# Performance work log

Hardware: AMD Instinct MI355X
Metric: run time of the kernel (lower is better)

## Reference

```python
import jax, jax.numpy as jnp
import numpy as np

BATCH = 8192
N = 32
A_NUM = 5
EPS = 1e-10
ALPHA = jnp.array([0.01, 0.25, 0.5, 0.9, 0.99], dtype=jnp.float32)


def setup_inputs() -> dict:
    key = jax.random.key(0)
    ks = jax.random.split(key, 9)
    stdv = 1.0 / np.sqrt(N)
    u = lambda k, shape: jax.random.uniform(k, shape, jnp.float32, -stdv, stdv)
    L = N * (N - 1) // 2
    return {
        "inputs": jax.random.normal(ks[0], (BATCH, N, N), jnp.float32),
        "state": jax.random.normal(ks[1], (BATCH, A_NUM * N * N), jnp.float32),
        "WR_root": u(ks[2], (A_NUM,)),
        "Wt_root": u(ks[3], (1,)),
        "Wphi_root": u(ks[4], (1,)),
        "Ws_root": u(ks[5], (A_NUM,)),
        "Br": u(ks[6], (L, 1)),
        "Bt": u(ks[7], (L, 1)),
        "By": u(ks[8], (L, 1)),
    }


def _skew(Bvec, n):
    # Replicates the torch loop: row 0 is zeros; row k (k>=1) gets B[k-1 : 2k-1]
    # in its first k columns (overlapping slices of the flat parameter vector).
    b = Bvec.reshape(-1)
    r = jnp.arange(n)[:, None]
    c = jnp.arange(n)[None, :]
    idx = jnp.clip(r - 1 + c, 0, b.shape[0] - 1)  # B[k-1+j] for entry (k, j)
    L = jnp.where(c < r, b[idx], jnp.zeros((), b.dtype))
    return L - L.T


def _cayley(S, n):
    # MatrixExp in the source: (I - S)^{-1} (I + S)
    I = jnp.eye(n, dtype=S.dtype)
    return jnp.linalg.solve(I - S, I + S)


def _translate(A, Bvec, n):
    # M @ A @ M.T with M the Cayley 'exp' of the skew matrix built from Bvec.
    M = _cayley(_skew(Bvec, n), n)
    return jnp.einsum('ij,bjk,lk->bil', M, A, M)


def _nus(W_root, A, eps):
    # Weighted average over the a_num axis with weights W_root^2 / (sum + eps).
    W = W_root * W_root
    return jnp.einsum('a,banm->bnm', W / (W.sum() + eps), A)


def reference(inputs, state, WR_root, Wt_root, Wphi_root, Ws_root, Br, Bt, By):
    Mt_1 = state.reshape(-1, A_NUM, N, N)                 # [B, a, n, n]
    X = inputs.reshape(BATCH, N, N)                       # [B, n, n]

    Yt = _nus(WR_root, Mt_1, EPS)                         # [B, n, n]
    Rt = _translate(Yt, Br, N)

    at = (Wt_root[0] ** 2) / ((Wt_root ** 2 + Wphi_root ** 2).sum() + EPS)
    Tt = (1.0 - at) * X + at * Rt                         # Frechet mean FM
    Phit = _translate(Tt, Bt, N)

    # Per-j Frechet means, vectorized over the a_num axis.
    a = ALPHA[None, :, None, None]
    Mt = (1.0 - a) * Mt_1 + a * Phit[:, None, :, :]       # [B, a, n, n]

    St = _nus(Ws_root, Mt, EPS)
    Ot = _translate(St, By, N)                            # [B, n, n]

    return Ot, Mt.reshape(-1, A_NUM, N, N)
```

## Files before the change

kernel.cpp:

```cpp
#include <hip/hip_runtime.h>

#define NB 8192
#define OT_ELEMS (NB * 1024)
#define EPSF 1e-10f

typedef __attribute__((ext_vector_type(4))) float f32x4;
typedef __attribute__((ext_vector_type(8))) short s16x8;

#define WAVE_FENCE() asm volatile("s_waitcnt lgkmcnt(0)" ::: "memory")
#define MFMA_B16(A, B, C) __builtin_amdgcn_mfma_f32_16x16x32_bf16((A), (B), (C), 0, 0, 0)

__global__ void cayley_kernel(const float* __restrict__ Br,
                              const float* __restrict__ Bt,
                              const float* __restrict__ By,
                              float* __restrict__ M_out) {
  __shared__ float A[32][33];
  __shared__ float R[32][33];
  const float* B = (blockIdx.x == 0) ? Br : (blockIdx.x == 1) ? Bt : By;
  const int t = threadIdx.x;
  const int i = t >> 5, j = t & 31;
  float Lij = (j < i) ? B[i - 1 + j] : 0.0f;
  float Lji = (i < j) ? B[j - 1 + i] : 0.0f;
  float S = Lij - Lji;
  float eye = (i == j) ? 1.0f : 0.0f;
  A[i][j] = eye - S;
  R[i][j] = eye + S;
  __syncthreads();
  for (int p = 0; p < 32; ++p) {
    float f = A[i][p] / A[p][p];
    __syncthreads();
    if (i != p) {
      A[i][j] -= f * A[p][j];
      R[i][j] -= f * R[p][j];
    }
    __syncthreads();
  }
  M_out[blockIdx.x * 1024 + i * 32 + j] = R[i][j] / A[i][i];
}

__device__ __forceinline__ void cvt_hilo8(const f32x4 f0, const f32x4 f1, s16x8& hi, s16x8& lo) {
  float f[8];
#pragma unroll
  for (int e = 0; e < 4; ++e) { f[e] = f0[e]; f[4 + e] = f1[e]; }
#pragma unroll
  for (int e = 0; e < 8; ++e) {
    unsigned u = __float_as_uint(f[e]);
    hi[e] = (short)(u >> 16);
    float ah = __uint_as_float(u & 0xffff0000u);
    lo[e] = (short)(__float_as_uint(f[e] - ah) >> 16);
  }
}

__device__ __forceinline__ void read_frag_lds(const float* sb, int off, s16x8& hi, s16x8& lo) {
  f32x4 f0 = *(const f32x4*)(sb + off);
  f32x4 f1 = *(const f32x4*)(sb + off + 4);
  cvt_hilo8(f0, f1, hi, lo);
}

__device__ __forceinline__ void congruence(float* sb, int lane,
                                           const s16x8 (&Mh)[2], const s16x8 (&Ml)[2],
                                           const f32x4 (&in)[2][2], f32x4 (&out)[2][2]) {
  const int l15 = lane & 15, l4 = lane >> 4;
#pragma unroll
  for (int ms = 0; ms < 2; ++ms)
#pragma unroll
    for (int ns = 0; ns < 2; ++ns)
      *(f32x4*)(sb + (16 * ns + l15) * 36 + 16 * ms + 4 * l4) = in[ms][ns];
  WAVE_FENCE();
  s16x8 Bh[2], Bl[2];
#pragma unroll
  for (int s = 0; s < 2; ++s)
    read_frag_lds(sb, (16 * s + l15) * 36 + 8 * l4, Bh[s], Bl[s]);
  WAVE_FENCE();
  f32x4 g[2][2];
#pragma unroll
  for (int ms = 0; ms < 2; ++ms)
#pragma unroll
    for (int ns = 0; ns < 2; ++ns) {
      f32x4 acc = {0.f, 0.f, 0.f, 0.f};
      acc = MFMA_B16(Ml[ms], Bh[ns], acc);
      acc = MFMA_B16(Mh[ms], Bl[ns], acc);
      acc = MFMA_B16(Mh[ms], Bh[ns], acc);
      g[ms][ns] = acc;
    }
#pragma unroll
  for (int ms = 0; ms < 2; ++ms)
#pragma unroll
    for (int ns = 0; ns < 2; ++ns)
#pragma unroll
      for (int r = 0; r < 4; ++r)
        sb[(16 * ms + 4 * l4 + r) * 36 + 16 * ns + l15] = g[ms][ns][r];
  WAVE_FENCE();
  s16x8 Ah[2], Al[2];
#pragma unroll
  for (int s = 0; s < 2; ++s)
    read_frag_lds(sb, (16 * s + l15) * 36 + 8 * l4, Ah[s], Al[s]);
  WAVE_FENCE();
#pragma unroll
  for (int ms = 0; ms < 2; ++ms)
#pragma unroll
    for (int ns = 0; ns < 2; ++ns) {
      f32x4 acc = {0.f, 0.f, 0.f, 0.f};
      acc = MFMA_B16(Al[ms], Mh[ns], acc);
      acc = MFMA_B16(Ah[ms], Ml[ns], acc);
      acc = MFMA_B16(Ah[ms], Mh[ns], acc);
      out[ms][ns] = acc;
    }
}

__global__ __launch_bounds__(64) void spdsru_main(
    const float* __restrict__ X, const float* __restrict__ state,
    const float* __restrict__ WR, const float* __restrict__ Wt,
    const float* __restrict__ Wphi, const float* __restrict__ Ws,
    const float* __restrict__ Mg, float* __restrict__ out) {
  __shared__ __align__(16) float sb[1152];
  const int lane = threadIdx.x;
  const int l15 = lane & 15, l4 = lane >> 4;
  const int batch = blockIdx.x;

  s16x8 Mh[3][2], Ml[3][2];
#pragma unroll
  for (int q = 0; q < 3; ++q)
#pragma unroll
    for (int s = 0; s < 2; ++s) {
      const float* p = Mg + q * 1024 + (16 * s + l15) * 32 + 8 * l4;
      cvt_hilo8(*(const f32x4*)p, *(const f32x4*)(p + 4), Mh[q][s], Ml[q][s]);
    }

  const float* xp = X + (size_t)batch * 1024;
  f32x4 x[2][2];
#pragma unroll
  for (int ms = 0; ms < 2; ++ms)
#pragma unroll
    for (int ns = 0; ns < 2; ++ns)
#pragma unroll
      for (int r = 0; r < 4; ++r)
        x[ms][ns][r] = xp[(16 * ms + 4 * l4 + r) * 32 + 16 * ns + l15];

  const float* stp = state + (size_t)batch * 5120;
  f32x4 m[5][2][2];
#pragma unroll
  for (int a = 0; a < 5; ++a)
#pragma unroll
    for (int ms = 0; ms < 2; ++ms)
#pragma unroll
      for (int ns = 0; ns < 2; ++ns)
#pragma unroll
        for (int r = 0; r < 4; ++r)
          m[a][ms][ns][r] = stp[a * 1024 + (16 * ms + 4 * l4 + r) * 32 + 16 * ns + l15];

  const float alpha[5] = {0.01f, 0.25f, 0.5f, 0.9f, 0.99f};
  float wr[5], wsn[5];
  {
    float sR = 0.f, sS = 0.f;
#pragma unroll
    for (int a = 0; a < 5; ++a) { float v = WR[a]; wr[a] = v * v; sR += v * v; }
#pragma unroll
    for (int a = 0; a < 5; ++a) { float v = Ws[a]; wsn[a] = v * v; sS += v * v; }
    const float invR = 1.0f / (sR + EPSF), invS = 1.0f / (sS + EPSF);
#pragma unroll
    for (int a = 0; a < 5; ++a) { wr[a] *= invR; wsn[a] *= invS; }
  }
  const float wt2 = Wt[0] * Wt[0], wp2 = Wphi[0] * Wphi[0];
  const float at = wt2 / (wt2 + wp2 + EPSF);
  const float omat = 1.0f - at;

  f32x4 U[2][2];
#pragma unroll
  for (int ms = 0; ms < 2; ++ms)
#pragma unroll
    for (int ns = 0; ns < 2; ++ns) {
      f32x4 u = wr[0] * m[0][ms][ns];
#pragma unroll
      for (int a = 1; a < 5; ++a) u += wr[a] * m[a][ms][ns];
      U[ms][ns] = u;
    }

  f32x4 rt[2][2];
  congruence(sb, lane, Mh[0], Ml[0], U, rt);

  f32x4 tt[2][2];
#pragma unroll
  for (int ms = 0; ms < 2; ++ms)
#pragma unroll
    for (int ns = 0; ns < 2; ++ns) tt[ms][ns] = omat * x[ms][ns] + at * rt[ms][ns];

  f32x4 ph[2][2];
  congruence(sb, lane, Mh[1], Ml[1], tt, ph);

  float* outMt = out + OT_ELEMS + (size_t)batch * 5120;
  f32x4 st[2][2];
#pragma unroll
  for (int ms = 0; ms < 2; ++ms)
#pragma unroll
    for (int ns = 0; ns < 2; ++ns) st[ms][ns] = f32x4{0.f, 0.f, 0.f, 0.f};
#pragma unroll
  for (int a = 0; a < 5; ++a) {
    const float al = alpha[a], om = 1.0f - al;
#pragma unroll
    for (int ms = 0; ms < 2; ++ms)
#pragma unroll
      for (int ns = 0; ns < 2; ++ns) {
        f32x4 mt = om * m[a][ms][ns] + al * ph[ms][ns];
        st[ms][ns] += wsn[a] * mt;
#pragma unroll
        for (int r = 0; r < 4; ++r)
          outMt[a * 1024 + (16 * ms + 4 * l4 + r) * 32 + 16 * ns + l15] = mt[r];
      }
  }

  f32x4 ot[2][2];
  congruence(sb, lane, Mh[2], Ml[2], st, ot);

  float* outOt = out + (size_t)batch * 1024;
#pragma unroll
  for (int ms = 0; ms < 2; ++ms)
#pragma unroll
    for (int ns = 0; ns < 2; ++ns)
#pragma unroll
      for (int r = 0; r < 4; ++r)
        outOt[(16 * ms + 4 * l4 + r) * 32 + 16 * ns + l15] = ot[ms][ns][r];
}

extern "C" void kernel_launch(void* const* d_in, const int* in_sizes, int n_in,
                              void* d_out, int out_size, void* d_ws, size_t ws_size,
                              hipStream_t stream) {
  const float* X     = (const float*)d_in[0];
  const float* state = (const float*)d_in[1];
  const float* WR    = (const float*)d_in[2];
  const float* Wt    = (const float*)d_in[3];
  const float* Wphi  = (const float*)d_in[4];
  const float* Ws    = (const float*)d_in[5];
  const float* Br    = (const float*)d_in[6];
  const float* Bt    = (const float*)d_in[7];
  const float* By    = (const float*)d_in[8];
  float* m_ws = (float*)d_ws;
  float* outp = (float*)d_out;

  cayley_kernel<<<3, 1024, 0, stream>>>(Br, Bt, By, m_ws);
  spdsru_main<<<NB, 64, 0, stream>>>(X, state, WR, Wt, Wphi, Ws, m_ws, outp);
}
```

Measured before the change: 104.9 us.

## Use 4x4 register tiles with vectorized global IO and fold St weights algebraically

Changes the per-lane ownership of each 32x32 matrix from the MFMA accumulator layout to a 4x4 tile, so global loads and stores become 16-byte vector accesses. The congruence routine now transposes through LDS on entry and exit to convert between this tile layout and the MFMA layout. The weighted sum St is rewritten as a precomputed weighted sum of the state plus a scalar times Phi. The state is read again from global memory in the Mt loop rather than kept in registers, which lowers register pressure but adds a second read and extra LDS round trips.

```diff
diff --git a/kernel.cpp b/kernel.cpp
--- a/kernel.cpp
+++ b/kernel.cpp
@@ -57,15 +57,16 @@
   cvt_hilo8(f0, f1, hi, lo);
 }
 
-__device__ __forceinline__ void congruence(float* sb, int lane,
-                                           const s16x8 (&Mh)[2], const s16x8 (&Ml)[2],
-                                           const f32x4 (&in)[2][2], f32x4 (&out)[2][2]) {
+__device__ __forceinline__ void congruence_rt(float* sb, int lane,
+                                              const s16x8 (&Mh)[2], const s16x8 (&Ml)[2],
+                                              const f32x4 (&in)[4], f32x4 (&outr)[4]) {
   const int l15 = lane & 15, l4 = lane >> 4;
-#pragma unroll
-  for (int ms = 0; ms < 2; ++ms)
-#pragma unroll
-    for (int ns = 0; ns < 2; ++ns)
-      *(f32x4*)(sb + (16 * ns + l15) * 36 + 16 * ms + 4 * l4) = in[ms][ns];
+  const int i0 = (lane >> 3) << 2, j0 = (lane & 7) << 2;
+#pragma unroll
+  for (int c = 0; c < 4; ++c) {
+    f32x4 colv = {in[0][c], in[1][c], in[2][c], in[3][c]};
+    *(f32x4*)(sb + (j0 + c) * 36 + i0) = colv;
+  }
   WAVE_FENCE();
   s16x8 Bh[2], Bl[2];
 #pragma unroll
@@ -96,6 +97,7 @@
   for (int s = 0; s < 2; ++s)
     read_frag_lds(sb, (16 * s + l15) * 36 + 8 * l4, Ah[s], Al[s]);
   WAVE_FENCE();
+  f32x4 o[2][2];
 #pragma unroll
   for (int ms = 0; ms < 2; ++ms)
 #pragma unroll
@@ -104,8 +106,20 @@
       acc = MFMA_B16(Al[ms], Mh[ns], acc);
       acc = MFMA_B16(Ah[ms], Ml[ns], acc);
       acc = MFMA_B16(Ah[ms], Mh[ns], acc);
-      out[ms][ns] = acc;
-    }
+      o[ms][ns] = acc;
+    }
+#pragma unroll
+  for (int ms = 0; ms < 2; ++ms)
+#pragma unroll
+    for (int ns = 0; ns < 2; ++ns)
+#pragma unroll
+      for (int r = 0; r < 4; ++r)
+        sb[(16 * ms + 4 * l4 + r) * 36 + 16 * ns + l15] = o[ms][ns][r];
+  WAVE_FENCE();
+#pragma unroll
+  for (int r = 0; r < 4; ++r)
+    outr[r] = *(const f32x4*)(sb + (i0 + r) * 36 + j0);
+  WAVE_FENCE();
 }
 
 __global__ __launch_bounds__(64) void spdsru_main(
@@ -116,6 +130,7 @@
   __shared__ __align__(16) float sb[1152];
   const int lane = threadIdx.x;
   const int l15 = lane & 15, l4 = lane >> 4;
+  const int i0 = (lane >> 3) << 2, j0 = (lane & 7) << 2;
   const int batch = blockIdx.x;
 
   s16x8 Mh[3][2], Ml[3][2];
@@ -127,99 +142,77 @@
       cvt_hilo8(*(const f32x4*)p, *(const f32x4*)(p + 4), Mh[q][s], Ml[q][s]);
     }
 
-  const float* xp = X + (size_t)batch * 1024;
-  f32x4 x[2][2];
-#pragma unroll
-  for (int ms = 0; ms < 2; ++ms)
-#pragma unroll
-    for (int ns = 0; ns < 2; ++ns)
-#pragma unroll
-      for (int r = 0; r < 4; ++r)
-        x[ms][ns][r] = xp[(16 * ms + 4 * l4 + r) * 32 + 16 * ns + l15];
-
-  const float* stp = state + (size_t)batch * 5120;
-  f32x4 m[5][2][2];
-#pragma unroll
-  for (int a = 0; a < 5; ++a)
-#pragma unroll
-    for (int ms = 0; ms < 2; ++ms)
-#pragma unroll
-      for (int ns = 0; ns < 2; ++ns)
-#pragma unroll
-        for (int r = 0; r < 4; ++r)
-          m[a][ms][ns][r] = stp[a * 1024 + (16 * ms + 4 * l4 + r) * 32 + 16 * ns + l15];
-
   const float alpha[5] = {0.01f, 0.25f, 0.5f, 0.9f, 0.99f};
-  float wr[5], wsn[5];
+  float wr[5], va[5];
+  float cP = 0.f;
   {
-    float sR = 0.f, sS = 0.f;
+    float sR = 0.f, sS = 0.f, wq[5];
 #pragma unroll
     for (int a = 0; a < 5; ++a) { float v = WR[a]; wr[a] = v * v; sR += v * v; }
 #pragma unroll
-    for (int a = 0; a < 5; ++a) { float v = Ws[a]; wsn[a] = v * v; sS += v * v; }
+    for (int a = 0; a < 5; ++a) { float v = Ws[a]; wq[a] = v * v; sS += v * v; }
     const float invR = 1.0f / (sR + EPSF), invS = 1.0f / (sS + EPSF);
 #pragma unroll
-    for (int a = 0; a < 5; ++a) { wr[a] *= invR; wsn[a] *= invS; }
+    for (int a = 0; a < 5; ++a) {
+      wr[a] *= invR;
+      float w = wq[a] * invS;
+      va[a] = w * (1.0f - alpha[a]);
+      cP += w * alpha[a];
+    }
   }
   const float wt2 = Wt[0] * Wt[0], wp2 = Wphi[0] * Wphi[0];
   const float at = wt2 / (wt2 + wp2 + EPSF);
   const float omat = 1.0f - at;
 
-  f32x4 U[2][2];
-#pragma unroll
-  for (int ms = 0; ms < 2; ++ms)
-#pragma unroll
-    for (int ns = 0; ns < 2; ++ns) {
-      f32x4 u = wr[0] * m[0][ms][ns];
-#pragma unroll
-      for (int a = 1; a < 5; ++a) u += wr[a] * m[a][ms][ns];
-      U[ms][ns] = u;
-    }
-
-  f32x4 rt[2][2];
-  congruence(sb, lane, Mh[0], Ml[0], U, rt);
-
-  f32x4 tt[2][2];
-#pragma unroll
-  for (int ms = 0; ms < 2; ++ms)
-#pragma unroll
-    for (int ns = 0; ns < 2; ++ns) tt[ms][ns] = omat * x[ms][ns] + at * rt[ms][ns];
-
-  f32x4 ph[2][2];
-  congruence(sb, lane, Mh[1], Ml[1], tt, ph);
+  const float* xp = X + (size_t)batch * 1024;
+  f32x4 x[4];
+#pragma unroll
+  for (int r = 0; r < 4; ++r) x[r] = *(const f32x4*)(xp + (i0 + r) * 32 + j0);
+
+  const float* stp = state + (size_t)batch * 5120;
+  f32x4 U[4], V[4];
+#pragma unroll
+  for (int r = 0; r < 4; ++r) { U[r] = f32x4{0.f, 0.f, 0.f, 0.f}; V[r] = U[r]; }
+#pragma unroll
+  for (int a = 0; a < 5; ++a)
+#pragma unroll
+    for (int r = 0; r < 4; ++r) {
+      const f32x4 v = *(const f32x4*)(stp + a * 1024 + (i0 + r) * 32 + j0);
+      U[r] += wr[a] * v;
+      V[r] += va[a] * v;
+    }
+
+  f32x4 rt[4];
+  congruence_rt(sb, lane, Mh[0], Ml[0], U, rt);
+  f32x4 tt[4];
+#pragma unroll
+  for (int r = 0; r < 4; ++r) tt[r] = omat * x[r] + at * rt[r];
+
+  f32x4 ph[4];
+  congruence_rt(sb, lane, Mh[1], Ml[1], tt, ph);
 
   float* outMt = out + OT_ELEMS + (size_t)batch * 5120;
-  f32x4 st[2][2];
-#pragma unroll
-  for (int ms = 0; ms < 2; ++ms)
-#pragma unroll
-    for (int ns = 0; ns < 2; ++ns) st[ms][ns] = f32x4{0.f, 0.f, 0.f, 0.f};
 #pragma unroll
   for (int a = 0; a < 5; ++a) {
     const float al = alpha[a], om = 1.0f - al;
 #pragma unroll
-    for (int ms = 0; ms < 2; ++ms)
-#pragma unroll
-      for (int ns = 0; ns < 2; ++ns) {
-        f32x4 mt = om * m[a][ms][ns] + al * ph[ms][ns];
-        st[ms][ns] += wsn[a] * mt;
-#pragma unroll
-        for (int r = 0; r < 4; ++r)
-          outMt[a * 1024 + (16 * ms + 4 * l4 + r) * 32 + 16 * ns + l15] = mt[r];
-      }
-  }
-
-  f32x4 ot[2][2];
-  congruence(sb, lane, Mh[2], Ml[2], st, ot);
+    for (int r = 0; r < 4; ++r) {
+      const f32x4 v = *(const f32x4*)(stp + a * 1024 + (i0 + r) * 32 + j0);
+      f32x4 w = om * v + al * ph[r];
+      *(f32x4*)(outMt + a * 1024 + (i0 + r) * 32 + j0) = w;
+    }
+  }
+
+  f32x4 st[4];
+#pragma unroll
+  for (int r = 0; r < 4; ++r) st[r] = V[r] + cP * ph[r];
+  f32x4 ot[4];
+  congruence_rt(sb, lane, Mh[2], Ml[2], st, ot);
 
   float* outOt = out + (size_t)batch * 1024;
 #pragma unroll
-  for (int ms = 0; ms < 2; ++ms)
-#pragma unroll
-    for (int ns = 0; ns < 2; ++ns)
-#pragma unroll
-      for (int r = 0; r < 4; ++r)
-        outOt[(16 * ms + 4 * l4 + r) * 32 + 16 * ns + l15] = ot[ms][ns][r];
+  for (int r = 0; r < 4; ++r)
+    *(f32x4*)(outOt + (i0 + r) * 32 + j0) = ot[r];
 }
 
 extern "C" void kernel_launch(void* const* d_in, const int* in_sizes, int n_in,
```

After: 101.4 us. -3.4%, faster.
